# Performance work log

Measured on AMD Instinct MI355X. Metric: run time of the kernel, lower is better.

The kernel has to match this reference:

```python
import jax, jax.numpy as jnp
import numpy as np

HIDDEN = 1024
MOE_FF = 512
SHARED_FF = 2816
NUM_EXPERTS = 16
TOP_K = 2
NORM_TOPK = True


def setup_inputs() -> dict:
    key = jax.random.key(0)
    ks = jax.random.split(key, 8)
    s = 0.02
    return {
        "layer_input": jax.random.normal(ks[0], (1, 2048, HIDDEN), dtype=jnp.float32),
        "gate_w": jax.random.normal(ks[1], (NUM_EXPERTS, HIDDEN), dtype=jnp.float32) * s,
        # fused gate_up weight per expert, laid out for x @ W: [E, hidden, 2*moe_ff]
        "w_gate_up": jax.random.normal(ks[2], (NUM_EXPERTS, HIDDEN, 2 * MOE_FF), dtype=jnp.float32) * s,
        # down weight per expert, laid out for h @ W: [E, moe_ff, hidden]
        "w_down": jax.random.normal(ks[3], (NUM_EXPERTS, MOE_FF, HIDDEN), dtype=jnp.float32) * s,
        # shared expert (Qwen2MoeMLP): Linear weights stored torch-style [out, in]
        "shared_w_gate": jax.random.normal(ks[4], (SHARED_FF, HIDDEN), dtype=jnp.float32) * s,
        "shared_w_up": jax.random.normal(ks[5], (SHARED_FF, HIDDEN), dtype=jnp.float32) * s,
        "shared_w_down": jax.random.normal(ks[6], (HIDDEN, SHARED_FF), dtype=jnp.float32) * s,
        "shared_gate_w": jax.random.normal(ks[7], (1, HIDDEN), dtype=jnp.float32) * s,
    }


def reference(layer_input, gate_w, w_gate_up, w_down,
              shared_w_gate, shared_w_up, shared_w_down, shared_gate_w):
    B, S, D = layer_input.shape
    x = layer_input.reshape(-1, D)  # [N, D]
    N = x.shape[0]

    # shared expert: silu-gated MLP, scaled by per-token sigmoid gate
    shared = (jax.nn.silu(x @ shared_w_gate.T) * (x @ shared_w_up.T)) @ shared_w_down.T
    shared = shared * jax.nn.sigmoid(x @ shared_gate_w.T)  # [N, D]

    # router: softmax in float32, top-k, optional renorm
    logits = x @ gate_w.T  # [N, E]
    probs = jax.nn.softmax(logits.astype(jnp.float32), axis=-1)
    rw, sel = jax.lax.top_k(probs, TOP_K)  # [N, K]
    if NORM_TOPK:
        rw = rw / rw.sum(axis=-1, keepdims=True)
    rw = rw.astype(x.dtype)

    # dense combine weights: zero for unselected experts (equivalent to
    # the sort/dispatch + grouped-GEMM + weighted scatter-combine)
    combine = jnp.zeros((N, NUM_EXPERTS), x.dtype).at[jnp.arange(N)[:, None], sel].set(rw)

    # expert gate_up projection, SwiGLU, down projection, weighted combine
    gu = jnp.einsum('nd,edf->nef', x, w_gate_up)  # [N, E, 2*moe_ff]
    g, h = jnp.split(gu, 2, axis=-1)
    h = jax.nn.silu(g) * h  # [N, E, moe_ff]
    expert_out = jnp.einsum('nef,efd,ne->nd', h, w_down, combine)  # [N, D]

    out = expert_out + shared
    return out.reshape(B, S, D)
```

## Files before the change

kernel.cpp:

```cpp
#include <hip/hip_runtime.h>
#include <hip/hip_bf16.h>

typedef unsigned short ushort_t;
typedef __bf16 bf16x8 __attribute__((ext_vector_type(8)));
typedef float f32x4 __attribute__((ext_vector_type(4)));

#define N_TOK 2048
#define DH    1024
#define FF    512
#define SFF   2816
#define NE    16

#define BM 128
#define BN 64
#define BK 64
#define LDK 72

__device__ __forceinline__ ushort_t f2bf(float f) {
  unsigned int x = __float_as_uint(f);
  unsigned int lsb = (x >> 16) & 1u;
  x += 0x7fffu + lsb;
  return (ushort_t)(x >> 16);
}

__device__ __forceinline__ uint4 cvt8v(const float4 a, const float4 b) {
  union { ushort_t u[8]; uint4 v; } r;
  r.u[0] = f2bf(a.x); r.u[1] = f2bf(a.y); r.u[2] = f2bf(a.z); r.u[3] = f2bf(a.w);
  r.u[4] = f2bf(b.x); r.u[5] = f2bf(b.y); r.u[6] = f2bf(b.z); r.u[7] = f2bf(b.w);
  return r.v;
}

__global__ void zero_acc_kernel(float4* __restrict__ acc) {
  acc[(size_t)blockIdx.x * 256 + threadIdx.x] = make_float4(0.f, 0.f, 0.f, 0.f);
}

__global__ void out_epilogue_kernel(const float4* __restrict__ acc, float4* __restrict__ out) {
  size_t i = (size_t)blockIdx.x * 256 + threadIdx.x;
  out[i] = acc[i];
}

__global__ void router_kernel(const float* __restrict__ X, const float* __restrict__ GW,
                              const float* __restrict__ SGW,
                              int* __restrict__ sel, float* __restrict__ wtk,
                              float* __restrict__ sgate) {
  int wave = threadIdx.x >> 6, lane = threadIdx.x & 63;
  int n = blockIdx.x * 4 + wave;
  const float* x = X + (size_t)n * DH;
  int e = lane & 15, s = lane >> 4;
  const float* gw = GW + (size_t)e * DH;
  float lg = 0.f;
  for (int i = 0; i < 256; ++i) {
    int d = s * 256 + i;
    lg += x[d] * gw[d];
  }
  lg += __shfl_down(lg, 32);
  lg += __shfl_down(lg, 16);

  float gd = 0.f;
  #pragma unroll
  for (int i = 0; i < 16; ++i) {
    int d = lane * 16 + i;
    gd += x[d] * SGW[d];
  }
  #pragma unroll
  for (int off = 32; off >= 1; off >>= 1) gd += __shfl_down(gd, off);

  float l[16];
  #pragma unroll
  for (int i = 0; i < 16; ++i) l[i] = __shfl(lg, i);

  if (lane == 0) {
    int i1 = 0; float v1 = l[0];
    #pragma unroll
    for (int i = 1; i < 16; ++i) if (l[i] > v1) { v1 = l[i]; i1 = i; }
    int i2 = -1; float v2 = -1e30f;
    #pragma unroll
    for (int i = 0; i < 16; ++i) { if (i == i1) continue; if (l[i] > v2) { v2 = l[i]; i2 = i; } }
    float p2 = __expf(v2 - v1);
    float inv = 1.f / (1.f + p2);
    sel[n * 2 + 0] = i1; sel[n * 2 + 1] = i2;
    wtk[n * 2 + 0] = inv; wtk[n * 2 + 1] = p2 * inv;
    sgate[n] = 1.f / (1.f + __expf(-gd));
  }
}

__global__ void scatter_kernel(const int* __restrict__ sel, const float* __restrict__ wtk,
                               int* __restrict__ toks, float* __restrict__ wts,
                               int* __restrict__ offs) {
  __shared__ int cnt[NE], bas[NE];
  int t = threadIdx.x;
  if (t < NE) cnt[t] = 0;
  __syncthreads();
  for (int i = t; i < N_TOK * 2; i += 256) atomicAdd(&cnt[sel[i]], 1);
  __syncthreads();
  if (t == 0) {
    int s = 0;
    for (int e = 0; e < NE; ++e) { bas[e] = s; offs[e] = s; s += cnt[e]; }
    offs[NE] = s;
  }
  __syncthreads();
  if (t < NE) cnt[t] = 0;
  __syncthreads();
  for (int i = t; i < N_TOK * 2; i += 256) {
    int e = sel[i];
    int p = atomicAdd(&cnt[e], 1);
    int slot = bas[e] + p;
    toks[slot] = i >> 1;
    wts[slot]  = wtk[i];
  }
}

__global__ __launch_bounds__(256, 2) void gateup_expert_kernel(
    const float* __restrict__ X, const float* __restrict__ WGU,
    ushort_t* __restrict__ H, const int* __restrict__ toks,
    const int* __restrict__ offs) {
  __shared__ __align__(16) ushort_t As[BM][LDK];
  __shared__ __align__(16) ushort_t Bgs[BN][LDK];
  __shared__ __align__(16) ushort_t Bus[BN][LDK];
  const int K = DH, NT = K / BK;

  int e = blockIdx.z;
  int base = offs[e], M = offs[e + 1] - base;
  int m0 = blockIdx.y * BM;
  if (m0 >= M) return;
  int n0 = blockIdx.x * BN;
  const float* W = WGU + (size_t)e * DH * (2 * FF);

  int t = threadIdx.x;
  int wave = t >> 6, lane = t & 63;
  int wm = wave & 1, wn = wave >> 1;
  int qd = lane >> 4, l16 = lane & 15;
  int sr = t >> 3, sc = (t & 7) * 8;
  int tn = t & 63, tk = (t >> 6) * 16;

  const float* arow[4];
  #pragma unroll
  for (int p = 0; p < 4; ++p) {
    int m = m0 + sr + 32 * p;
    int mm = m < M ? m : (M - 1);
    arow[p] = X + (size_t)toks[base + mm] * K + sc;
  }
  const float* wkb = W + (size_t)tk * (2 * FF) + n0 + tn;

  float4 ar[4][2];
  float bgr[16], bur[16];
  #pragma unroll
  for (int p = 0; p < 4; ++p) {
    ar[p][0] = *(const float4*)(arow[p]);
    ar[p][1] = *(const float4*)(arow[p] + 4);
  }
  #pragma unroll
  for (int j = 0; j < 16; ++j) {
    bgr[j] = wkb[(size_t)j * (2 * FF)];
    bur[j] = wkb[(size_t)j * (2 * FF) + FF];
  }

  f32x4 accg[4][2], accu[4][2];
  #pragma unroll
  for (int i = 0; i < 4; ++i)
    #pragma unroll
    for (int j = 0; j < 2; ++j) {
      accg[i][j] = (f32x4){0.f, 0.f, 0.f, 0.f};
      accu[i][j] = (f32x4){0.f, 0.f, 0.f, 0.f};
    }

  for (int kt = 0; kt < NT; ++kt) {
    #pragma unroll
    for (int p = 0; p < 4; ++p)
      *(uint4*)&As[sr + 32 * p][sc] = cvt8v(ar[p][0], ar[p][1]);
    {
      union { ushort_t u[8]; uint4 v; } g0, g1, u0, u1;
      #pragma unroll
      for (int j = 0; j < 8; ++j) {
        g0.u[j] = f2bf(bgr[j]); g1.u[j] = f2bf(bgr[8 + j]);
        u0.u[j] = f2bf(bur[j]); u1.u[j] = f2bf(bur[8 + j]);
      }
      *(uint4*)&Bgs[tn][tk]     = g0.v;
      *(uint4*)&Bgs[tn][tk + 8] = g1.v;
      *(uint4*)&Bus[tn][tk]     = u0.v;
      *(uint4*)&Bus[tn][tk + 8] = u1.v;
    }
    __syncthreads();
    if (kt + 1 < NT) {
      int ko = (kt + 1) * BK;
      #pragma unroll
      for (int p = 0; p < 4; ++p) {
        ar[p][0] = *(const float4*)(arow[p] + ko);
        ar[p][1] = *(const float4*)(arow[p] + ko + 4);
      }
      const float* wk = wkb + (size_t)ko * (2 * FF);
      #pragma unroll
      for (int j = 0; j < 16; ++j) {
        bgr[j] = wk[(size_t)j * (2 * FF)];
        bur[j] = wk[(size_t)j * (2 * FF) + FF];
      }
    }
    #pragma unroll
    for (int ks = 0; ks < 2; ++ks) {
      int kk = ks * 32 + qd * 8;
      bf16x8 af[4], bgf[2], buf[2];
      #pragma unroll
      for (int i = 0; i < 4; ++i)
        af[i] = *(const bf16x8*)&As[wm * 64 + i * 16 + l16][kk];
      #pragma unroll
      for (int j = 0; j < 2; ++j) {
        bgf[j] = *(const bf16x8*)&Bgs[wn * 32 + j * 16 + l16][kk];
        buf[j] = *(const bf16x8*)&Bus[wn * 32 + j * 16 + l16][kk];
      }
      #pragma unroll
      for (int i = 0; i < 4; ++i)
        #pragma unroll
        for (int j = 0; j < 2; ++j) {
          accg[i][j] = __builtin_amdgcn_mfma_f32_16x16x32_bf16(af[i], bgf[j], accg[i][j], 0, 0, 0);
          accu[i][j] = __builtin_amdgcn_mfma_f32_16x16x32_bf16(af[i], buf[j], accu[i][j], 0, 0, 0);
        }
    }
    __syncthreads();
  }

  #pragma unroll
  for (int i = 0; i < 4; ++i)
    #pragma unroll
    for (int r = 0; r < 4; ++r) {
      int m = m0 + wm * 64 + i * 16 + qd * 4 + r;
      if (m >= M) continue;
      #pragma unroll
      for (int j = 0; j < 2; ++j) {
        float g = accg[i][j][r], u = accu[i][j][r];
        float h = g / (1.f + __expf(-g)) * u;
        int col = n0 + wn * 32 + j * 16 + l16;
        H[(size_t)(base + m) * FF + col] = f2bf(h);
      }
    }
}

__global__ __launch_bounds__(256, 2) void gateup_shared_kernel(
    const float* __restrict__ X, const float* __restrict__ Bg,
    const float* __restrict__ Bu, ushort_t* __restrict__ H) {
  __shared__ __align__(16) ushort_t As[BM][LDK];
  __shared__ __align__(16) ushort_t Bgs[BN][LDK];
  __shared__ __align__(16) ushort_t Bus[BN][LDK];
  const int K = DH, NT = K / BK;

  int m0 = blockIdx.y * BM;
  int n0 = blockIdx.x * BN;
  int t = threadIdx.x;
  int wave = t >> 6, lane = t & 63;
  int wm = wave & 1, wn = wave >> 1;
  int qd = lane >> 4, l16 = lane & 15;
  int sr = t >> 3, sc = (t & 7) * 8;

  const float* arow[4];
  const float *bgrow[2], *burow[2];
  #pragma unroll
  for (int p = 0; p < 4; ++p)
    arow[p] = X + (size_t)(m0 + sr + 32 * p) * K + sc;
  #pragma unroll
  for (int p = 0; p < 2; ++p) {
    bgrow[p] = Bg + (size_t)(n0 + sr + 32 * p) * K + sc;
    burow[p] = Bu + (size_t)(n0 + sr + 32 * p) * K + sc;
  }

  float4 ar[4][2], bgr[2][2], bur[2][2];
  #pragma unroll
  for (int p = 0; p < 4; ++p) {
    ar[p][0] = *(const float4*)(arow[p]);
    ar[p][1] = *(const float4*)(arow[p] + 4);
  }
  #pragma unroll
  for (int p = 0; p < 2; ++p) {
    bgr[p][0] = *(const float4*)(bgrow[p]);
    bgr[p][1] = *(const float4*)(bgrow[p] + 4);
    bur[p][0] = *(const float4*)(burow[p]);
    bur[p][1] = *(const float4*)(burow[p] + 4);
  }

  f32x4 accg[4][2], accu[4][2];
  #pragma unroll
  for (int i = 0; i < 4; ++i)
    #pragma unroll
    for (int j = 0; j < 2; ++j) {
      accg[i][j] = (f32x4){0.f, 0.f, 0.f, 0.f};
      accu[i][j] = (f32x4){0.f, 0.f, 0.f, 0.f};
    }

  for (int kt = 0; kt < NT; ++kt) {
    #pragma unroll
    for (int p = 0; p < 4; ++p)
      *(uint4*)&As[sr + 32 * p][sc] = cvt8v(ar[p][0], ar[p][1]);
    #pragma unroll
    for (int p = 0; p < 2; ++p) {
      *(uint4*)&Bgs[sr + 32 * p][sc] = cvt8v(bgr[p][0], bgr[p][1]);
      *(uint4*)&Bus[sr + 32 * p][sc] = cvt8v(bur[p][0], bur[p][1]);
    }
    __syncthreads();
    if (kt + 1 < NT) {
      int ko = (kt + 1) * BK;
      #pragma unroll
      for (int p = 0; p < 4; ++p) {
        ar[p][0] = *(const float4*)(arow[p] + ko);
        ar[p][1] = *(const float4*)(arow[p] + ko + 4);
      }
      #pragma unroll
      for (int p = 0; p < 2; ++p) {
        bgr[p][0] = *(const float4*)(bgrow[p] + ko);
        bgr[p][1] = *(const float4*)(bgrow[p] + ko + 4);
        bur[p][0] = *(const float4*)(burow[p] + ko);
        bur[p][1] = *(const float4*)(burow[p] + ko + 4);
      }
    }
    #pragma unroll
    for (int ks = 0; ks < 2; ++ks) {
      int kk = ks * 32 + qd * 8;
      bf16x8 af[4], bgf[2], buf[2];
      #pragma unroll
      for (int i = 0; i < 4; ++i)
        af[i] = *(const bf16x8*)&As[wm * 64 + i * 16 + l16][kk];
      #pragma unroll
      for (int j = 0; j < 2; ++j) {
        bgf[j] = *(const bf16x8*)&Bgs[wn * 32 + j * 16 + l16][kk];
        buf[j] = *(const bf16x8*)&Bus[wn * 32 + j * 16 + l16][kk];
      }
      #pragma unroll
      for (int i = 0; i < 4; ++i)
        #pragma unroll
        for (int j = 0; j < 2; ++j) {
          accg[i][j] = __builtin_amdgcn_mfma_f32_16x16x32_bf16(af[i], bgf[j], accg[i][j], 0, 0, 0);
          accu[i][j] = __builtin_amdgcn_mfma_f32_16x16x32_bf16(af[i], buf[j], accu[i][j], 0, 0, 0);
        }
    }
    __syncthreads();
  }

  #pragma unroll
  for (int i = 0; i < 4; ++i)
    #pragma unroll
    for (int r = 0; r < 4; ++r) {
      int m = m0 + wm * 64 + i * 16 + qd * 4 + r;
      #pragma unroll
      for (int j = 0; j < 2; ++j) {
        float g = accg[i][j][r], u = accu[i][j][r];
        float h = g / (1.f + __expf(-g)) * u;
        int col = n0 + wn * 32 + j * 16 + l16;
        H[(size_t)m * SFF + col] = f2bf(h);
      }
    }
}

__global__ __launch_bounds__(256, 2) void down_expert_kernel(
    const ushort_t* __restrict__ HX, const float* __restrict__ WDN,
    float* __restrict__ acc, const int* __restrict__ toks,
    const float* __restrict__ wts, const int* __restrict__ offs) {
  __shared__ __align__(16) ushort_t As[BM][LDK];
  __shared__ __align__(16) ushort_t Bs[BN][LDK];
  const int K = FF, NT = K / BK;

  int e = blockIdx.z;
  int base = offs[e], M = offs[e + 1] - base;
  int m0 = blockIdx.y * BM;
  if (m0 >= M) return;
  int n0 = blockIdx.x * BN;
  const float* W = WDN + (size_t)e * FF * DH;
  const ushort_t* A = HX + (size_t)base * K;

  int t = threadIdx.x;
  int wave = t >> 6, lane = t & 63;
  int wm = wave & 1, wn = wave >> 1;
  int qd = lane >> 4, l16 = lane & 15;
  int sr = t >> 3, sc = (t & 7) * 8;
  int tn = t & 63, tk = (t >> 6) * 16;

  const ushort_t* arow[4];
  #pragma unroll
  for (int p = 0; p < 4; ++p)
    arow[p] = A + (size_t)(m0 + sr + 32 * p) * K + sc;
  const float* wkb = W + (size_t)tk * DH + n0 + tn;

  uint4 ar[4];
  float br[16];
  #pragma unroll
  for (int p = 0; p < 4; ++p) ar[p] = *(const uint4*)(arow[p]);
  #pragma unroll
  for (int j = 0; j < 16; ++j) br[j] = wkb[(size_t)j * DH];

  f32x4 c[4][2];
  #pragma unroll
  for (int i = 0; i < 4; ++i)
    #pragma unroll
    for (int j = 0; j < 2; ++j) c[i][j] = (f32x4){0.f, 0.f, 0.f, 0.f};

  for (int kt = 0; kt < NT; ++kt) {
    #pragma unroll
    for (int p = 0; p < 4; ++p)
      *(uint4*)&As[sr + 32 * p][sc] = ar[p];
    {
      union { ushort_t u[8]; uint4 v; } b0, b1;
      #pragma unroll
      for (int j = 0; j < 8; ++j) { b0.u[j] = f2bf(br[j]); b1.u[j] = f2bf(br[8 + j]); }
      *(uint4*)&Bs[tn][tk]     = b0.v;
      *(uint4*)&Bs[tn][tk + 8] = b1.v;
    }
    __syncthreads();
    if (kt + 1 < NT) {
      int ko = (kt + 1) * BK;
      #pragma unroll
      for (int p = 0; p < 4; ++p) ar[p] = *(const uint4*)(arow[p] + ko);
      const float* wk = wkb + (size_t)ko * DH;
      #pragma unroll
      for (int j = 0; j < 16; ++j) br[j] = wk[(size_t)j * DH];
    }
    #pragma unroll
    for (int ks = 0; ks < 2; ++ks) {
      int kk = ks * 32 + qd * 8;
      bf16x8 af[4], bf[2];
      #pragma unroll
      for (int i = 0; i < 4; ++i)
        af[i] = *(const bf16x8*)&As[wm * 64 + i * 16 + l16][kk];
      #pragma unroll
      for (int j = 0; j < 2; ++j)
        bf[j] = *(const bf16x8*)&Bs[wn * 32 + j * 16 + l16][kk];
      #pragma unroll
      for (int i = 0; i < 4; ++i)
        #pragma unroll
        for (int j = 0; j < 2; ++j)
          c[i][j] = __builtin_amdgcn_mfma_f32_16x16x32_bf16(af[i], bf[j], c[i][j], 0, 0, 0);
    }
    __syncthreads();
  }

  #pragma unroll
  for (int i = 0; i < 4; ++i)
    #pragma unroll
    for (int r = 0; r < 4; ++r) {
      int m = m0 + wm * 64 + i * 16 + qd * 4 + r;
      if (m >= M) continue;
      int tok = toks[base + m];
      float w = wts[base + m];
      #pragma unroll
      for (int j = 0; j < 2; ++j) {
        int n = n0 + wn * 32 + j * 16 + l16;
        atomicAdd(&acc[(size_t)tok * DH + n], c[i][j][r] * w);
      }
    }
}

__global__ __launch_bounds__(256, 2) void down_shared_kernel(
    const ushort_t* __restrict__ HS, const float* __restrict__ Bp,
    float* __restrict__ acc, const float* __restrict__ sgate) {
  __shared__ __align__(16) ushort_t As[BM][LDK];
  __shared__ __align__(16) ushort_t Bs[BN][LDK];
  const int KC = SFF / 2, NT = KC / BK;

  int m0 = blockIdx.y * BM;
  int n0 = blockIdx.x * BN;
  int kb = blockIdx.z * KC;
  int t = threadIdx.x;
  int wave = t >> 6, lane = t & 63;
  int wm = wave & 1, wn = wave >> 1;
  int qd = lane >> 4, l16 = lane & 15;
  int sr = t >> 3, sc = (t & 7) * 8;

  const ushort_t* arow[4];
  const float* brow[2];
  #pragma unroll
  for (int p = 0; p < 4; ++p)
    arow[p] = HS + (size_t)(m0 + sr + 32 * p) * SFF + kb + sc;
  #pragma unroll
  for (int p = 0; p < 2; ++p)
    brow[p] = Bp + (size_t)(n0 + sr + 32 * p) * SFF + kb + sc;

  uint4 ar[4];
  float4 br[2][2];
  #pragma unroll
  for (int p = 0; p < 4; ++p) ar[p] = *(const uint4*)(arow[p]);
  #pragma unroll
  for (int p = 0; p < 2; ++p) {
    br[p][0] = *(const float4*)(brow[p]);
    br[p][1] = *(const float4*)(brow[p] + 4);
  }

  f32x4 c[4][2];
  #pragma unroll
  for (int i = 0; i < 4; ++i)
    #pragma unroll
    for (int j = 0; j < 2; ++j) c[i][j] = (f32x4){0.f, 0.f, 0.f, 0.f};

  for (int kt = 0; kt < NT; ++kt) {
    #pragma unroll
    for (int p = 0; p < 4; ++p)
      *(uint4*)&As[sr + 32 * p][sc] = ar[p];
    #pragma unroll
    for (int p = 0; p < 2; ++p)
      *(uint4*)&Bs[sr + 32 * p][sc] = cvt8v(br[p][0], br[p][1]);
    __syncthreads();
    if (kt + 1 < NT) {
      int ko = (kt + 1) * BK;
      #pragma unroll
      for (int p = 0; p < 4; ++p) ar[p] = *(const uint4*)(arow[p] + ko);
      #pragma unroll
      for (int p = 0; p < 2; ++p) {
        br[p][0] = *(const float4*)(brow[p] + ko);
        br[p][1] = *(const float4*)(brow[p] + ko + 4);
      }
    }
    #pragma unroll
    for (int ks = 0; ks < 2; ++ks) {
      int kk = ks * 32 + qd * 8;
      bf16x8 af[4], bf[2];
      #pragma unroll
      for (int i = 0; i < 4; ++i)
        af[i] = *(const bf16x8*)&As[wm * 64 + i * 16 + l16][kk];
      #pragma unroll
      for (int j = 0; j < 2; ++j)
        bf[j] = *(const bf16x8*)&Bs[wn * 32 + j * 16 + l16][kk];
      #pragma unroll
      for (int i = 0; i < 4; ++i)
        #pragma unroll
        for (int j = 0; j < 2; ++j)
          c[i][j] = __builtin_amdgcn_mfma_f32_16x16x32_bf16(af[i], bf[j], c[i][j], 0, 0, 0);
    }
    __syncthreads();
  }

  #pragma unroll
  for (int i = 0; i < 4; ++i)
    #pragma unroll
    for (int r = 0; r < 4; ++r) {
      int m = m0 + wm * 64 + i * 16 + qd * 4 + r;
      float sg = sgate[m];
      #pragma unroll
      for (int j = 0; j < 2; ++j) {
        int n = n0 + wn * 32 + j * 16 + l16;
        atomicAdd(&acc[(size_t)m * DH + n], c[i][j][r] * sg);
      }
    }
}

extern "C" void kernel_launch(void* const* d_in, const int* in_sizes, int n_in,
                              void* d_out, int out_size, void* d_ws, size_t ws_size,
                              hipStream_t stream) {
  const float* x    = (const float*)d_in[0];
  const float* gw   = (const float*)d_in[1];
  const float* wgu  = (const float*)d_in[2];
  const float* wdn  = (const float*)d_in[3];
  const float* swg  = (const float*)d_in[4];
  const float* swu  = (const float*)d_in[5];
  const float* swd  = (const float*)d_in[6];
  const float* sgw  = (const float*)d_in[7];
  float* out = (float*)d_out;

  char* ws = (char*)d_ws;
  constexpr size_t OFF_ACC  = 0;
  constexpr size_t OFF_HS   = OFF_ACC + (size_t)N_TOK * DH * 4;
  constexpr size_t OFF_HX   = OFF_HS  + (size_t)N_TOK * SFF * 2;
  constexpr size_t OFF_TOK  = OFF_HX  + (size_t)4224 * FF * 2;
  constexpr size_t OFF_WTS  = OFF_TOK + 4224 * 4;
  constexpr size_t OFF_OFFS = OFF_WTS + 4224 * 4;
  constexpr size_t OFF_SEL  = OFF_OFFS + 32 * 4;
  constexpr size_t OFF_WTK  = OFF_SEL + 4096 * 4;
  constexpr size_t OFF_SG   = OFF_WTK + 4096 * 4;

  float*    acc   = (float*)(ws + OFF_ACC);
  ushort_t* hs    = (ushort_t*)(ws + OFF_HS);
  ushort_t* hx    = (ushort_t*)(ws + OFF_HX);
  int*      toks  = (int*)(ws + OFF_TOK);
  float*    wts   = (float*)(ws + OFF_WTS);
  int*      offs  = (int*)(ws + OFF_OFFS);
  int*      sel   = (int*)(ws + OFF_SEL);
  float*    wtk   = (float*)(ws + OFF_WTK);
  float*    sgate = (float*)(ws + OFF_SG);

  zero_acc_kernel<<<2048, 256, 0, stream>>>((float4*)acc);
  router_kernel<<<N_TOK / 4, 256, 0, stream>>>(x, gw, sgw, sel, wtk, sgate);
  scatter_kernel<<<1, 256, 0, stream>>>(sel, wtk, toks, wts, offs);
  gateup_expert_kernel<<<dim3(FF / BN, 16, NE), 256, 0, stream>>>(
      x, wgu, hx, toks, offs);
  gateup_shared_kernel<<<dim3(SFF / BN, N_TOK / BM, 1), 256, 0, stream>>>(
      x, swg, swu, hs);
  down_expert_kernel<<<dim3(DH / BN, 16, NE), 256, 0, stream>>>(
      hx, wdn, acc, toks, wts, offs);
  down_shared_kernel<<<dim3(DH / BN, N_TOK / BM, 2), 256, 0, stream>>>(
      hs, swd, acc, sgate);
  out_epilogue_kernel<<<2048, 256, 0, stream>>>((const float4*)acc, (float4*)out);
}
```

Measured before the change: 410.3 us.

## Merge expert and shared GEMMs into combined launches and fold zeroing into router

The expert and shared gate-up GEMMs now run in one launch with a flat block index that picks the branch, and the expert and shared down GEMMs likewise share one launch. Zeroing the accumulator moves into the router kernel, which removes a separate launch. Global loads now convert to bf16 as they arrive, so fp32 staging registers shrink, and the launch-bounds occupancy hints rise to 3 and 4 blocks. This cuts launch count and lets expert and shared work fill the GPU together, at the cost of higher register pressure under the tighter bounds.

```diff
diff --git a/kernel.cpp b/kernel.cpp
--- a/kernel.cpp
+++ b/kernel.cpp
@@ -30,8 +30,10 @@
   return r.v;
 }
 
-__global__ void zero_acc_kernel(float4* __restrict__ acc) {
-  acc[(size_t)blockIdx.x * 256 + threadIdx.x] = make_float4(0.f, 0.f, 0.f, 0.f);
+__device__ __forceinline__ uint4 ld_cvt8(const float* __restrict__ p) {
+  float4 a = *(const float4*)p;
+  float4 b = *(const float4*)(p + 4);
+  return cvt8v(a, b);
 }
 
 __global__ void out_epilogue_kernel(const float4* __restrict__ acc, float4* __restrict__ out) {
@@ -42,7 +44,12 @@
 __global__ void router_kernel(const float* __restrict__ X, const float* __restrict__ GW,
                               const float* __restrict__ SGW,
                               int* __restrict__ sel, float* __restrict__ wtk,
-                              float* __restrict__ sgate) {
+                              float* __restrict__ sgate, float4* __restrict__ accv) {
+  {
+    size_t b0 = (size_t)blockIdx.x * 1024 + threadIdx.x;
+    float4 z = make_float4(0.f, 0.f, 0.f, 0.f);
+    accv[b0] = z; accv[b0 + 256] = z; accv[b0 + 512] = z; accv[b0 + 768] = z;
+  }
   int wave = threadIdx.x >> 6, lane = threadIdx.x & 63;
   int n = blockIdx.x * 4 + wave;
   const float* x = X + (size_t)n * DH;
@@ -110,430 +117,389 @@
   }
 }
 
-__global__ __launch_bounds__(256, 2) void gateup_expert_kernel(
+__global__ __launch_bounds__(256, 3) void gateup_kernel(
     const float* __restrict__ X, const float* __restrict__ WGU,
-    ushort_t* __restrict__ H, const int* __restrict__ toks,
-    const int* __restrict__ offs) {
+    const float* __restrict__ Bg, const float* __restrict__ Bu,
+    ushort_t* __restrict__ HX, ushort_t* __restrict__ HS,
+    const int* __restrict__ toks, const int* __restrict__ offs) {
   __shared__ __align__(16) ushort_t As[BM][LDK];
   __shared__ __align__(16) ushort_t Bgs[BN][LDK];
   __shared__ __align__(16) ushort_t Bus[BN][LDK];
   const int K = DH, NT = K / BK;
 
-  int e = blockIdx.z;
-  int base = offs[e], M = offs[e + 1] - base;
-  int m0 = blockIdx.y * BM;
-  if (m0 >= M) return;
-  int n0 = blockIdx.x * BN;
-  const float* W = WGU + (size_t)e * DH * (2 * FF);
-
+  int bid = blockIdx.x;
   int t = threadIdx.x;
   int wave = t >> 6, lane = t & 63;
   int wm = wave & 1, wn = wave >> 1;
   int qd = lane >> 4, l16 = lane & 15;
   int sr = t >> 3, sc = (t & 7) * 8;
-  int tn = t & 63, tk = (t >> 6) * 16;
-
-  const float* arow[4];
-  #pragma unroll
-  for (int p = 0; p < 4; ++p) {
-    int m = m0 + sr + 32 * p;
-    int mm = m < M ? m : (M - 1);
-    arow[p] = X + (size_t)toks[base + mm] * K + sc;
-  }
-  const float* wkb = W + (size_t)tk * (2 * FF) + n0 + tn;
-
-  float4 ar[4][2];
-  float bgr[16], bur[16];
-  #pragma unroll
-  for (int p = 0; p < 4; ++p) {
-    ar[p][0] = *(const float4*)(arow[p]);
-    ar[p][1] = *(const float4*)(arow[p] + 4);
-  }
-  #pragma unroll
-  for (int j = 0; j < 16; ++j) {
-    bgr[j] = wkb[(size_t)j * (2 * FF)];
-    bur[j] = wkb[(size_t)j * (2 * FF) + FF];
-  }
-
-  f32x4 accg[4][2], accu[4][2];
-  #pragma unroll
-  for (int i = 0; i < 4; ++i)
-    #pragma unroll
-    for (int j = 0; j < 2; ++j) {
-      accg[i][j] = (f32x4){0.f, 0.f, 0.f, 0.f};
-      accu[i][j] = (f32x4){0.f, 0.f, 0.f, 0.f};
-    }
-
-  for (int kt = 0; kt < NT; ++kt) {
+
+  if (bid < 2048) {
+    int e = bid >> 7, rem = bid & 127;
+    int n0 = (rem & 7) * BN, m0 = (rem >> 3) * BM;
+    int base = offs[e], M = offs[e + 1] - base;
+    if (m0 >= M) return;
+    const float* W = WGU + (size_t)e * DH * (2 * FF);
+    int tn = t & 63, tk = (t >> 6) * 16;
+
+    const float* arow[4];
+    #pragma unroll
+    for (int p = 0; p < 4; ++p) {
+      int m = m0 + sr + 32 * p;
+      int mm = m < M ? m : (M - 1);
+      arow[p] = X + (size_t)toks[base + mm] * K + sc;
+    }
+    const float* wkb = W + (size_t)tk * (2 * FF) + n0 + tn;
+
+    uint4 ar[4];
+    float bgr[16], bur[16];
+    #pragma unroll
+    for (int p = 0; p < 4; ++p) ar[p] = ld_cvt8(arow[p]);
+    #pragma unroll
+    for (int j = 0; j < 16; ++j) {
+      bgr[j] = wkb[(size_t)j * (2 * FF)];
+      bur[j] = wkb[(size_t)j * (2 * FF) + FF];
+    }
+
+    f32x4 accg[4][2], accu[4][2];
+    #pragma unroll
+    for (int i = 0; i < 4; ++i)
+      #pragma unroll
+      for (int j = 0; j < 2; ++j) {
+        accg[i][j] = (f32x4){0.f, 0.f, 0.f, 0.f};
+        accu[i][j] = (f32x4){0.f, 0.f, 0.f, 0.f};
+      }
+
+    for (int kt = 0; kt < NT; ++kt) {
+      #pragma unroll
+      for (int p = 0; p < 4; ++p)
+        *(uint4*)&As[sr + 32 * p][sc] = ar[p];
+      {
+        union { ushort_t u[8]; uint4 v; } g0, g1, u0, u1;
+        #pragma unroll
+        for (int j = 0; j < 8; ++j) {
+          g0.u[j] = f2bf(bgr[j]); g1.u[j] = f2bf(bgr[8 + j]);
+          u0.u[j] = f2bf(bur[j]); u1.u[j] = f2bf(bur[8 + j]);
+        }
+        *(uint4*)&Bgs[tn][tk]     = g0.v;
+        *(uint4*)&Bgs[tn][tk + 8] = g1.v;
+        *(uint4*)&Bus[tn][tk]     = u0.v;
+        *(uint4*)&Bus[tn][tk + 8] = u1.v;
+      }
+      __syncthreads();
+      if (kt + 1 < NT) {
+        int ko = (kt + 1) * BK;
+        #pragma unroll
+        for (int p = 0; p < 4; ++p) ar[p] = ld_cvt8(arow[p] + ko);
+        const float* wk = wkb + (size_t)ko * (2 * FF);
+        #pragma unroll
+        for (int j = 0; j < 16; ++j) {
+          bgr[j] = wk[(size_t)j * (2 * FF)];
+          bur[j] = wk[(size_t)j * (2 * FF) + FF];
+        }
+      }
+      #pragma unroll
+      for (int ks = 0; ks < 2; ++ks) {
+        int kk = ks * 32 + qd * 8;
+        bf16x8 af[4], bgf[2], buf[2];
+        #pragma unroll
+        for (int i = 0; i < 4; ++i)
+          af[i] = *(const bf16x8*)&As[wm * 64 + i * 16 + l16][kk];
+        #pragma unroll
+        for (int j = 0; j < 2; ++j) {
+          bgf[j] = *(const bf16x8*)&Bgs[wn * 32 + j * 16 + l16][kk];
+          buf[j] = *(const bf16x8*)&Bus[wn * 32 + j * 16 + l16][kk];
+        }
+        #pragma unroll
+        for (int i = 0; i < 4; ++i)
+          #pragma unroll
+          for (int j = 0; j < 2; ++j) {
+            accg[i][j] = __builtin_amdgcn_mfma_f32_16x16x32_bf16(af[i], bgf[j], accg[i][j], 0, 0, 0);
+            accu[i][j] = __builtin_amdgcn_mfma_f32_16x16x32_bf16(af[i], buf[j], accu[i][j], 0, 0, 0);
+          }
+      }
+      __syncthreads();
+    }
+
+    #pragma unroll
+    for (int i = 0; i < 4; ++i)
+      #pragma unroll
+      for (int r = 0; r < 4; ++r) {
+        int m = m0 + wm * 64 + i * 16 + qd * 4 + r;
+        if (m >= M) continue;
+        #pragma unroll
+        for (int j = 0; j < 2; ++j) {
+          float g = accg[i][j][r], u = accu[i][j][r];
+          float h = g / (1.f + __expf(-g)) * u;
+          int col = n0 + wn * 32 + j * 16 + l16;
+          HX[(size_t)(base + m) * FF + col] = f2bf(h);
+        }
+      }
+  } else {
+    unsigned s = bid - 2048;
+    int n0 = (int)(s % 44u) * BN, m0 = (int)(s / 44u) * BM;
+
+    const float* arow[4];
+    const float *bgrow[2], *burow[2];
     #pragma unroll
     for (int p = 0; p < 4; ++p)
-      *(uint4*)&As[sr + 32 * p][sc] = cvt8v(ar[p][0], ar[p][1]);
-    {
-      union { ushort_t u[8]; uint4 v; } g0, g1, u0, u1;
-      #pragma unroll
-      for (int j = 0; j < 8; ++j) {
-        g0.u[j] = f2bf(bgr[j]); g1.u[j] = f2bf(bgr[8 + j]);
-        u0.u[j] = f2bf(bur[j]); u1.u[j] = f2bf(bur[8 + j]);
-      }
-      *(uint4*)&Bgs[tn][tk]     = g0.v;
-      *(uint4*)&Bgs[tn][tk + 8] = g1.v;
-      *(uint4*)&Bus[tn][tk]     = u0.v;
-      *(uint4*)&Bus[tn][tk + 8] = u1.v;
-    }
-    __syncthreads();
-    if (kt + 1 < NT) {
-      int ko = (kt + 1) * BK;
-      #pragma unroll
-      for (int p = 0; p < 4; ++p) {
-        ar[p][0] = *(const float4*)(arow[p] + ko);
-        ar[p][1] = *(const float4*)(arow[p] + ko + 4);
-      }
-      const float* wk = wkb + (size_t)ko * (2 * FF);
-      #pragma unroll
-      for (int j = 0; j < 16; ++j) {
-        bgr[j] = wk[(size_t)j * (2 * FF)];
-        bur[j] = wk[(size_t)j * (2 * FF) + FF];
-      }
-    }
-    #pragma unroll
-    for (int ks = 0; ks < 2; ++ks) {
-      int kk = ks * 32 + qd * 8;
-      bf16x8 af[4], bgf[2], buf[2];
-      #pragma unroll
-      for (int i = 0; i < 4; ++i)
-        af[i] = *(const bf16x8*)&As[wm * 64 + i * 16 + l16][kk];
+      arow[p] = X + (size_t)(m0 + sr + 32 * p) * K + sc;
+    #pragma unroll
+    for (int p = 0; p < 2; ++p) {
+      bgrow[p] = Bg + (size_t)(n0 + sr + 32 * p) * K + sc;
+      burow[p] = Bu + (size_t)(n0 + sr + 32 * p) * K + sc;
+    }
+
+    uint4 ar[4], bgr[2], bur[2];
+    #pragma unroll
+    for (int p = 0; p < 4; ++p) ar[p] = ld_cvt8(arow[p]);
+    #pragma unroll
+    for (int p = 0; p < 2; ++p) {
+      bgr[p] = ld_cvt8(bgrow[p]);
+      bur[p] = ld_cvt8(burow[p]);
+    }
+
+    f32x4 accg[4][2], accu[4][2];
+    #pragma unroll
+    for (int i = 0; i < 4; ++i)
       #pragma unroll
       for (int j = 0; j < 2; ++j) {
-        bgf[j] = *(const bf16x8*)&Bgs[wn * 32 + j * 16 + l16][kk];
-        buf[j] = *(const bf16x8*)&Bus[wn * 32 + j * 16 + l16][kk];
-      }
-      #pragma unroll
-      for (int i = 0; i < 4; ++i)
+        accg[i][j] = (f32x4){0.f, 0.f, 0.f, 0.f};
+        accu[i][j] = (f32x4){0.f, 0.f, 0.f, 0.f};
+      }
+
+    for (int kt = 0; kt < NT; ++kt) {
+      #pragma unroll
+      for (int p = 0; p < 4; ++p)
+        *(uint4*)&As[sr + 32 * p][sc] = ar[p];
+      #pragma unroll
+      for (int p = 0; p < 2; ++p) {
+        *(uint4*)&Bgs[sr + 32 * p][sc] = bgr[p];
+        *(uint4*)&Bus[sr + 32 * p][sc] = bur[p];
+      }
+      __syncthreads();
+      if (kt + 1 < NT) {
+        int ko = (kt + 1) * BK;
+        #pragma unroll
+        for (int p = 0; p < 4; ++p) ar[p] = ld_cvt8(arow[p] + ko);
+        #pragma unroll
+        for (int p = 0; p < 2; ++p) {
+          bgr[p] = ld_cvt8(bgrow[p] + ko);
+          bur[p] = ld_cvt8(burow[p] + ko);
+        }
+      }
+      #pragma unroll
+      for (int ks = 0; ks < 2; ++ks) {
+        int kk = ks * 32 + qd * 8;
+        bf16x8 af[4], bgf[2], buf[2];
+        #pragma unroll
+        for (int i = 0; i < 4; ++i)
+          af[i] = *(const bf16x8*)&As[wm * 64 + i * 16 + l16][kk];
         #pragma unroll
         for (int j = 0; j < 2; ++j) {
-          accg[i][j] = __builtin_amdgcn_mfma_f32_16x16x32_bf16(af[i], bgf[j], accg[i][j], 0, 0, 0);
-          accu[i][j] = __builtin_amdgcn_mfma_f32_16x16x32_bf16(af[i], buf[j], accu[i][j], 0, 0, 0);
-        }
-    }
-    __syncthreads();
-  }
-
-  #pragma unroll
-  for (int i = 0; i < 4; ++i)
-    #pragma unroll
-    for (int r = 0; r < 4; ++r) {
-      int m = m0 + wm * 64 + i * 16 + qd * 4 + r;
-      if (m >= M) continue;
-      #pragma unroll
-      for (int j = 0; j < 2; ++j) {
-        float g = accg[i][j][r], u = accu[i][j][r];
-        float h = g / (1.f + __expf(-g)) * u;
-        int col = n0 + wn * 32 + j * 16 + l16;
-        H[(size_t)(base + m) * FF + col] = f2bf(h);
-      }
-    }
-}
-
-__global__ __launch_bounds__(256, 2) void gateup_shared_kernel(
-    const float* __restrict__ X, const float* __restrict__ Bg,
-    const float* __restrict__ Bu, ushort_t* __restrict__ H) {
+          bgf[j] = *(const bf16x8*)&Bgs[wn * 32 + j * 16 + l16][kk];
+          buf[j] = *(const bf16x8*)&Bus[wn * 32 + j * 16 + l16][kk];
+        }
+        #pragma unroll
+        for (int i = 0; i < 4; ++i)
+          #pragma unroll
+          for (int j = 0; j < 2; ++j) {
+            accg[i][j] = __builtin_amdgcn_mfma_f32_16x16x32_bf16(af[i], bgf[j], accg[i][j], 0, 0, 0);
+            accu[i][j] = __builtin_amdgcn_mfma_f32_16x16x32_bf16(af[i], buf[j], accu[i][j], 0, 0, 0);
+          }
+      }
+      __syncthreads();
+    }
+
+    #pragma unroll
+    for (int i = 0; i < 4; ++i)
+      #pragma unroll
+      for (int r = 0; r < 4; ++r) {
+        int m = m0 + wm * 64 + i * 16 + qd * 4 + r;
+        #pragma unroll
+        for (int j = 0; j < 2; ++j) {
+          float g = accg[i][j][r], u = accu[i][j][r];
+          float h = g / (1.f + __expf(-g)) * u;
+          int col = n0 + wn * 32 + j * 16 + l16;
+          HS[(size_t)m * SFF + col] = f2bf(h);
+        }
+      }
+  }
+}
+
+__global__ __launch_bounds__(256, 4) void down_kernel(
+    const ushort_t* __restrict__ HX, const ushort_t* __restrict__ HS,
+    const float* __restrict__ WDN, const float* __restrict__ SWD,
+    float* __restrict__ acc, const int* __restrict__ toks,
+    const float* __restrict__ wts, const int* __restrict__ offs,
+    const float* __restrict__ sgate) {
   __shared__ __align__(16) ushort_t As[BM][LDK];
-  __shared__ __align__(16) ushort_t Bgs[BN][LDK];
-  __shared__ __align__(16) ushort_t Bus[BN][LDK];
-  const int K = DH, NT = K / BK;
-
-  int m0 = blockIdx.y * BM;
-  int n0 = blockIdx.x * BN;
+  __shared__ __align__(16) ushort_t Bs[BN][LDK];
+
+  int bid = blockIdx.x;
   int t = threadIdx.x;
   int wave = t >> 6, lane = t & 63;
   int wm = wave & 1, wn = wave >> 1;
   int qd = lane >> 4, l16 = lane & 15;
   int sr = t >> 3, sc = (t & 7) * 8;
 
-  const float* arow[4];
-  const float *bgrow[2], *burow[2];
-  #pragma unroll
-  for (int p = 0; p < 4; ++p)
-    arow[p] = X + (size_t)(m0 + sr + 32 * p) * K + sc;
-  #pragma unroll
-  for (int p = 0; p < 2; ++p) {
-    bgrow[p] = Bg + (size_t)(n0 + sr + 32 * p) * K + sc;
-    burow[p] = Bu + (size_t)(n0 + sr + 32 * p) * K + sc;
-  }
-
-  float4 ar[4][2], bgr[2][2], bur[2][2];
-  #pragma unroll
-  for (int p = 0; p < 4; ++p) {
-    ar[p][0] = *(const float4*)(arow[p]);
-    ar[p][1] = *(const float4*)(arow[p] + 4);
-  }
-  #pragma unroll
-  for (int p = 0; p < 2; ++p) {
-    bgr[p][0] = *(const float4*)(bgrow[p]);
-    bgr[p][1] = *(const float4*)(bgrow[p] + 4);
-    bur[p][0] = *(const float4*)(burow[p]);
-    bur[p][1] = *(const float4*)(burow[p] + 4);
-  }
-
-  f32x4 accg[4][2], accu[4][2];
-  #pragma unroll
-  for (int i = 0; i < 4; ++i)
-    #pragma unroll
-    for (int j = 0; j < 2; ++j) {
-      accg[i][j] = (f32x4){0.f, 0.f, 0.f, 0.f};
-      accu[i][j] = (f32x4){0.f, 0.f, 0.f, 0.f};
-    }
-
-  for (int kt = 0; kt < NT; ++kt) {
+  if (bid < 4096) {
+    int e = bid >> 8, rem = bid & 255;
+    int n0 = (rem & 15) * BN, m0 = (rem >> 4) * BM;
+    int base = offs[e], M = offs[e + 1] - base;
+    if (m0 >= M) return;
+    const int K = FF, NT = K / BK;
+    const float* W = WDN + (size_t)e * FF * DH;
+    const ushort_t* A = HX + (size_t)base * K;
+    int tn = t & 63, tk = (t >> 6) * 16;
+
+    const ushort_t* arow[4];
     #pragma unroll
     for (int p = 0; p < 4; ++p)
-      *(uint4*)&As[sr + 32 * p][sc] = cvt8v(ar[p][0], ar[p][1]);
-    #pragma unroll
-    for (int p = 0; p < 2; ++p) {
-      *(uint4*)&Bgs[sr + 32 * p][sc] = cvt8v(bgr[p][0], bgr[p][1]);
-      *(uint4*)&Bus[sr + 32 * p][sc] = cvt8v(bur[p][0], bur[p][1]);
-    }
-    __syncthreads();
-    if (kt + 1 < NT) {
-      int ko = (kt + 1) * BK;
-      #pragma unroll
-      for (int p = 0; p < 4; ++p) {
-        ar[p][0] = *(const float4*)(arow[p] + ko);
-        ar[p][1] = *(const float4*)(arow[p] + ko + 4);
-      }
-      #pragma unroll
-      for (int p = 0; p < 2; ++p) {
-        bgr[p][0] = *(const float4*)(bgrow[p] + ko);
-        bgr[p][1] = *(const float4*)(bgrow[p] + ko + 4);
-        bur[p][0] = *(const float4*)(burow[p] + ko);
-        bur[p][1] = *(const float4*)(burow[p] + ko + 4);
-      }
-    }
-    #pragma unroll
-    for (int ks = 0; ks < 2; ++ks) {
-      int kk = ks * 32 + qd * 8;
-      bf16x8 af[4], bgf[2], buf[2];
-      #pragma unroll
-      for (int i = 0; i < 4; ++i)
-        af[i] = *(const bf16x8*)&As[wm * 64 + i * 16 + l16][kk];
-      #pragma unroll
-      for (int j = 0; j < 2; ++j) {
-        bgf[j] = *(const bf16x8*)&Bgs[wn * 32 + j * 16 + l16][kk];
-        buf[j] = *(const bf16x8*)&Bus[wn * 32 + j * 16 + l16][kk];
-      }
-      #pragma unroll
-      for (int i = 0; i < 4; ++i)
+      arow[p] = A + (size_t)(m0 + sr + 32 * p) * K + sc;
+    const float* wkb = W + (size_t)tk * DH + n0 + tn;
+
+    uint4 ar[4];
+    float br[16];
+    #pragma unroll
+    for (int p = 0; p < 4; ++p) ar[p] = *(const uint4*)(arow[p]);
+    #pragma unroll
+    for (int j = 0; j < 16; ++j) br[j] = wkb[(size_t)j * DH];
+
+    f32x4 c[4][2];
+    #pragma unroll
+    for (int i = 0; i < 4; ++i)
+      #pragma unroll
+      for (int j = 0; j < 2; ++j) c[i][j] = (f32x4){0.f, 0.f, 0.f, 0.f};
+
+    for (int kt = 0; kt < NT; ++kt) {
+      #pragma unroll
+      for (int p = 0; p < 4; ++p)
+        *(uint4*)&As[sr + 32 * p][sc] = ar[p];
+      {
+        union { ushort_t u[8]; uint4 v; } b0, b1;
+        #pragma unroll
+        for (int j = 0; j < 8; ++j) { b0.u[j] = f2bf(br[j]); b1.u[j] = f2bf(br[8 + j]); }
+        *(uint4*)&Bs[tn][tk]     = b0.v;
+        *(uint4*)&Bs[tn][tk + 8] = b1.v;
+      }
+      __syncthreads();
+      if (kt + 1 < NT) {
+        int ko = (kt + 1) * BK;
+        #pragma unroll
+        for (int p = 0; p < 4; ++p) ar[p] = *(const uint4*)(arow[p] + ko);
+        const float* wk = wkb + (size_t)ko * DH;
+        #pragma unroll
+        for (int j = 0; j < 16; ++j) br[j] = wk[(size_t)j * DH];
+      }
+      #pragma unroll
+      for (int ks = 0; ks < 2; ++ks) {
+        int kk = ks * 32 + qd * 8;
+        bf16x8 af[4], bf[2];
+        #pragma unroll
+        for (int i = 0; i < 4; ++i)
+          af[i] = *(const bf16x8*)&As[wm * 64 + i * 16 + l16][kk];
+        #pragma unroll
+        for (int j = 0; j < 2; ++j)
+          bf[j] = *(const bf16x8*)&Bs[wn * 32 + j * 16 + l16][kk];
+        #pragma unroll
+        for (int i = 0; i < 4; ++i)
+          #pragma unroll
+          for (int j = 0; j < 2; ++j)
+            c[i][j] = __builtin_amdgcn_mfma_f32_16x16x32_bf16(af[i], bf[j], c[i][j], 0, 0, 0);
+      }
+      __syncthreads();
+    }
+
+    #pragma unroll
+    for (int i = 0; i < 4; ++i)
+      #pragma unroll
+      for (int r = 0; r < 4; ++r) {
+        int m = m0 + wm * 64 + i * 16 + qd * 4 + r;
+        if (m >= M) continue;
+        int tok = toks[base + m];
+        float w = wts[base + m];
         #pragma unroll
         for (int j = 0; j < 2; ++j) {
-          accg[i][j] = __builtin_amdgcn_mfma_f32_16x16x32_bf16(af[i], bgf[j], accg[i][j], 0, 0, 0);
-          accu[i][j] = __builtin_amdgcn_mfma_f32_16x16x32_bf16(af[i], buf[j], accu[i][j], 0, 0, 0);
-        }
-    }
-    __syncthreads();
-  }
-
-  #pragma unroll
-  for (int i = 0; i < 4; ++i)
-    #pragma unroll
-    for (int r = 0; r < 4; ++r) {
-      int m = m0 + wm * 64 + i * 16 + qd * 4 + r;
-      #pragma unroll
-      for (int j = 0; j < 2; ++j) {
-        float g = accg[i][j][r], u = accu[i][j][r];
-        float h = g / (1.f + __expf(-g)) * u;
-        int col = n0 + wn * 32 + j * 16 + l16;
-        H[(size_t)m * SFF + col] = f2bf(h);
-      }
-    }
-}
-
-__global__ __launch_bounds__(256, 2) void down_expert_kernel(
-    const ushort_t* __restrict__ HX, const float* __restrict__ WDN,
-    float* __restrict__ acc, const int* __restrict__ toks,
-    const float* __restrict__ wts, const int* __restrict__ offs) {
-  __shared__ __align__(16) ushort_t As[BM][LDK];
-  __shared__ __align__(16) ushort_t Bs[BN][LDK];
-  const int K = FF, NT = K / BK;
-
-  int e = blockIdx.z;
-  int base = offs[e], M = offs[e + 1] - base;
-  int m0 = blockIdx.y * BM;
-  if (m0 >= M) return;
-  int n0 = blockIdx.x * BN;
-  const float* W = WDN + (size_t)e * FF * DH;
-  const ushort_t* A = HX + (size_t)base * K;
-
-  int t = threadIdx.x;
-  int wave = t >> 6, lane = t & 63;
-  int wm = wave & 1, wn = wave >> 1;
-  int qd = lane >> 4, l16 = lane & 15;
-  int sr = t >> 3, sc = (t & 7) * 8;
-  int tn = t & 63, tk = (t >> 6) * 16;
-
-  const ushort_t* arow[4];
-  #pragma unroll
-  for (int p = 0; p < 4; ++p)
-    arow[p] = A + (size_t)(m0 + sr + 32 * p) * K + sc;
-  const float* wkb = W + (size_t)tk * DH + n0 + tn;
-
-  uint4 ar[4];
-  float br[16];
-  #pragma unroll
-  for (int p = 0; p < 4; ++p) ar[p] = *(const uint4*)(arow[p]);
-  #pragma unroll
-  for (int j = 0; j < 16; ++j) br[j] = wkb[(size_t)j * DH];
-
-  f32x4 c[4][2];
-  #pragma unroll
-  for (int i = 0; i < 4; ++i)
-    #pragma unroll
-    for (int j = 0; j < 2; ++j) c[i][j] = (f32x4){0.f, 0.f, 0.f, 0.f};
-
-  for (int kt = 0; kt < NT; ++kt) {
+          int n = n0 + wn * 32 + j * 16 + l16;
+          atomicAdd(&acc[(size_t)tok * DH + n], c[i][j][r] * w);
+        }
+      }
+  } else {
+    int s = bid - 4096;
+    int kz = s >> 8, rem = s & 255;
+    int n0 = (rem & 15) * BN, m0 = (rem >> 4) * BM;
+    const int KC = SFF / 2, NT = KC / BK;
+    int kb = kz * KC;
+
+    const ushort_t* arow[4];
+    const float* brow[2];
     #pragma unroll
     for (int p = 0; p < 4; ++p)
-      *(uint4*)&As[sr + 32 * p][sc] = ar[p];
-    {
-      union { ushort_t u[8]; uint4 v; } b0, b1;
-      #pragma unroll
-      for (int j = 0; j < 8; ++j) { b0.u[j] = f2bf(br[j]); b1.u[j] = f2bf(br[8 + j]); }
-      *(uint4*)&Bs[tn][tk]     = b0.v;
-      *(uint4*)&Bs[tn][tk + 8] = b1.v;
-    }
-    __syncthreads();
-    if (kt + 1 < NT) {
-      int ko = (kt + 1) * BK;
-      #pragma unroll
-      for (int p = 0; p < 4; ++p) ar[p] = *(const uint4*)(arow[p] + ko);
-      const float* wk = wkb + (size_t)ko * DH;
-      #pragma unroll
-      for (int j = 0; j < 16; ++j) br[j] = wk[(size_t)j * DH];
-    }
-    #pragma unroll
-    for (int ks = 0; ks < 2; ++ks) {
-      int kk = ks * 32 + qd * 8;
-      bf16x8 af[4], bf[2];
-      #pragma unroll
-      for (int i = 0; i < 4; ++i)
-        af[i] = *(const bf16x8*)&As[wm * 64 + i * 16 + l16][kk];
-      #pragma unroll
-      for (int j = 0; j < 2; ++j)
-        bf[j] = *(const bf16x8*)&Bs[wn * 32 + j * 16 + l16][kk];
-      #pragma unroll
-      for (int i = 0; i < 4; ++i)
+      arow[p] = HS + (size_t)(m0 + sr + 32 * p) * SFF + kb + sc;
+    #pragma unroll
+    for (int p = 0; p < 2; ++p)
+      brow[p] = SWD + (size_t)(n0 + sr + 32 * p) * SFF + kb + sc;
+
+    uint4 ar[4], br[2];
+    #pragma unroll
+    for (int p = 0; p < 4; ++p) ar[p] = *(const uint4*)(arow[p]);
+    #pragma unroll
+    for (int p = 0; p < 2; ++p) br[p] = ld_cvt8(brow[p]);
+
+    f32x4 c[4][2];
+    #pragma unroll
+    for (int i = 0; i < 4; ++i)
+      #pragma unroll
+      for (int j = 0; j < 2; ++j) c[i][j] = (f32x4){0.f, 0.f, 0.f, 0.f};
+
+    for (int kt = 0; kt < NT; ++kt) {
+      #pragma unroll
+      for (int p = 0; p < 4; ++p)
+        *(uint4*)&As[sr + 32 * p][sc] = ar[p];
+      #pragma unroll
+      for (int p = 0; p < 2; ++p)
+        *(uint4*)&Bs[sr + 32 * p][sc] = br[p];
+      __syncthreads();
+      if (kt + 1 < NT) {
+        int ko = (kt + 1) * BK;
+        #pragma unroll
+        for (int p = 0; p < 4; ++p) ar[p] = *(const uint4*)(arow[p] + ko);
+        #pragma unroll
+        for (int p = 0; p < 2; ++p) br[p] = ld_cvt8(brow[p] + ko);
+      }
+      #pragma unroll
+      for (int ks = 0; ks < 2; ++ks) {
+        int kk = ks * 32 + qd * 8;
+        bf16x8 af[4], bf[2];
+        #pragma unroll
+        for (int i = 0; i < 4; ++i)
+          af[i] = *(const bf16x8*)&As[wm * 64 + i * 16 + l16][kk];
         #pragma unroll
         for (int j = 0; j < 2; ++j)
-          c[i][j] = __builtin_amdgcn_mfma_f32_16x16x32_bf16(af[i], bf[j], c[i][j], 0, 0, 0);
-    }
-    __syncthreads();
-  }
-
-  #pragma unroll
-  for (int i = 0; i < 4; ++i)
-    #pragma unroll
-    for (int r = 0; r < 4; ++r) {
-      int m = m0 + wm * 64 + i * 16 + qd * 4 + r;
-      if (m >= M) continue;
-      int tok = toks[base + m];
-      float w = wts[base + m];
-      #pragma unroll
-      for (int j = 0; j < 2; ++j) {
-        int n = n0 + wn * 32 + j * 16 + l16;
-        atomicAdd(&acc[(size_t)tok * DH + n], c[i][j][r] * w);
-      }
-    }
-}
-
-__global__ __launch_bounds__(256, 2) void down_shared_kernel(
-    const ushort_t* __restrict__ HS, const float* __restrict__ Bp,
-    float* __restrict__ acc, const float* __restrict__ sgate) {
-  __shared__ __align__(16) ushort_t As[BM][LDK];
-  __shared__ __align__(16) ushort_t Bs[BN][LDK];
-  const int KC = SFF / 2, NT = KC / BK;
-
-  int m0 = blockIdx.y * BM;
-  int n0 = blockIdx.x * BN;
-  int kb = blockIdx.z * KC;
-  int t = threadIdx.x;
-  int wave = t >> 6, lane = t & 63;
-  int wm = wave & 1, wn = wave >> 1;
-  int qd = lane >> 4, l16 = lane & 15;
-  int sr = t >> 3, sc = (t & 7) * 8;
-
-  const ushort_t* arow[4];
-  const float* brow[2];
-  #pragma unroll
-  for (int p = 0; p < 4; ++p)
-    arow[p] = HS + (size_t)(m0 + sr + 32 * p) * SFF + kb + sc;
-  #pragma unroll
-  for (int p = 0; p < 2; ++p)
-    brow[p] = Bp + (size_t)(n0 + sr + 32 * p) * SFF + kb + sc;
-
-  uint4 ar[4];
-  float4 br[2][2];
-  #pragma unroll
-  for (int p = 0; p < 4; ++p) ar[p] = *(const uint4*)(arow[p]);
-  #pragma unroll
-  for (int p = 0; p < 2; ++p) {
-    br[p][0] = *(const float4*)(brow[p]);
-    br[p][1] = *(const float4*)(brow[p] + 4);
-  }
-
-  f32x4 c[4][2];
-  #pragma unroll
-  for (int i = 0; i < 4; ++i)
-    #pragma unroll
-    for (int j = 0; j < 2; ++j) c[i][j] = (f32x4){0.f, 0.f, 0.f, 0.f};
-
-  for (int kt = 0; kt < NT; ++kt) {
-    #pragma unroll
-    for (int p = 0; p < 4; ++p)
-      *(uint4*)&As[sr + 32 * p][sc] = ar[p];
-    #pragma unroll
-    for (int p = 0; p < 2; ++p)
-      *(uint4*)&Bs[sr + 32 * p][sc] = cvt8v(br[p][0], br[p][1]);
-    __syncthreads();
-    if (kt + 1 < NT) {
-      int ko = (kt + 1) * BK;
-      #pragma unroll
-      for (int p = 0; p < 4; ++p) ar[p] = *(const uint4*)(arow[p] + ko);
-      #pragma unroll
-      for (int p = 0; p < 2; ++p) {
-        br[p][0] = *(const float4*)(brow[p] + ko);
-        br[p][1] = *(const float4*)(brow[p] + ko + 4);
-      }
-    }
-    #pragma unroll
-    for (int ks = 0; ks < 2; ++ks) {
-      int kk = ks * 32 + qd * 8;
-      bf16x8 af[4], bf[2];
-      #pragma unroll
-      for (int i = 0; i < 4; ++i)
-        af[i] = *(const bf16x8*)&As[wm * 64 + i * 16 + l16][kk];
-      #pragma unroll
-      for (int j = 0; j < 2; ++j)
-        bf[j] = *(const bf16x8*)&Bs[wn * 32 + j * 16 + l16][kk];
-      #pragma unroll
-      for (int i = 0; i < 4; ++i)
-        #pragma unroll
-        for (int j = 0; j < 2; ++j)
-          c[i][j] = __builtin_amdgcn_mfma_f32_16x16x32_bf16(af[i], bf[j], c[i][j], 0, 0, 0);
-    }
-    __syncthreads();
-  }
-
-  #pragma unroll
-  for (int i = 0; i < 4; ++i)
-    #pragma unroll
-    for (int r = 0; r < 4; ++r) {
-      int m = m0 + wm * 64 + i * 16 + qd * 4 + r;
-      float sg = sgate[m];
-      #pragma unroll
-      for (int j = 0; j < 2; ++j) {
-        int n = n0 + wn * 32 + j * 16 + l16;
-        atomicAdd(&acc[(size_t)m * DH + n], c[i][j][r] * sg);
-      }
-    }
+          bf[j] = *(const bf16x8*)&Bs[wn * 32 + j * 16 + l16][kk];
+        #pragma unroll
+        for (int i = 0; i < 4; ++i)
+          #pragma unroll
+          for (int j = 0; j < 2; ++j)
+            c[i][j] = __builtin_amdgcn_mfma_f32_16x16x32_bf16(af[i], bf[j], c[i][j], 0, 0, 0);
+      }
+      __syncthreads();
+    }
+
+    #pragma unroll
+    for (int i = 0; i < 4; ++i)
+      #pragma unroll
+      for (int r = 0; r < 4; ++r) {
+        int m = m0 + wm * 64 + i * 16 + qd * 4 + r;
+        float sg = sgate[m];
+        #pragma unroll
+        for (int j = 0; j < 2; ++j) {
+          int n = n0 + wn * 32 + j * 16 + l16;
+          atomicAdd(&acc[(size_t)m * DH + n], c[i][j][r] * sg);
+        }
+      }
+  }
 }
 
 extern "C" void kernel_launch(void* const* d_in, const int* in_sizes, int n_in,
@@ -570,16 +536,9 @@
   float*    wtk   = (float*)(ws + OFF_WTK);
   float*    sgate = (float*)(ws + OFF_SG);
 
-  zero_acc_kernel<<<2048, 256, 0, stream>>>((float4*)acc);
-  router_kernel<<<N_TOK / 4, 256, 0, stream>>>(x, gw, sgw, sel, wtk, sgate);
+  router_kernel<<<N_TOK / 4, 256, 0, stream>>>(x, gw, sgw, sel, wtk, sgate, (float4*)acc);
   scatter_kernel<<<1, 256, 0, stream>>>(sel, wtk, toks, wts, offs);
-  gateup_expert_kernel<<<dim3(FF / BN, 16, NE), 256, 0, stream>>>(
-      x, wgu, hx, toks, offs);
-  gateup_shared_kernel<<<dim3(SFF / BN, N_TOK / BM, 1), 256, 0, stream>>>(
-      x, swg, swu, hs);
-  down_expert_kernel<<<dim3(DH / BN, 16, NE), 256, 0, stream>>>(
-      hx, wdn, acc, toks, wts, offs);
-  down_shared_kernel<<<dim3(DH / BN, N_TOK / BM, 2), 256, 0, stream>>>(
-      hs, swd, acc, sgate);
+  gateup_kernel<<<2048 + 704, 256, 0, stream>>>(x, wgu, swg, swu, hx, hs, toks, offs);
+  down_kernel<<<4096 + 512, 256, 0, stream>>>(hx, hs, wdn, swd, acc, toks, wts, offs, sgate);
   out_epilogue_kernel<<<2048, 256, 0, stream>>>((const float4*)acc, (float4*)out);
 }
```

New measurement: 436.7 us. 6.4% more time.
